# Performance work log

Hardware: AMD Instinct MI355X
Metric: run time of the kernel (lower is better)

Reference implementation:

```python
import jax, jax.numpy as jnp
import numpy as np

LN_EPS = 1e-5

def _lstm_scan(xp, w_hh):
    # xp: [T, B, 4H] precomputed input projections (+bias); w_hh: [4H, H]
    H = w_hh.shape[1]
    B = xp.shape[1]
    def step(carry, x_t):
        h, c = carry
        gates = x_t + h @ w_hh.T
        i, f, g, o = jnp.split(gates, 4, axis=-1)  # torch gate order i,f,g,o
        i = jax.nn.sigmoid(i); f = jax.nn.sigmoid(f)
        g = jnp.tanh(g); o = jax.nn.sigmoid(o)
        c = f * c + i * g
        h = o * jnp.tanh(c)
        return (h, c), h
    init = (jnp.zeros((B, H), xp.dtype), jnp.zeros((B, H), xp.dtype))
    _, hs = jax.lax.scan(step, init, xp)
    return hs  # [T, B, H]

def setup_inputs() -> dict:
    key = jax.random.key(0)
    ks = jax.random.split(key, 16)
    B, T, V, E, K = 64, 512, 21128, 256, 9
    H4 = 4 * E
    s = 0.08  # small init scale for numerical stability
    return {
        'word_ids': jax.random.randint(ks[0], (B, T), 0, V, dtype=jnp.int32),
        'label_ids': jax.random.randint(ks[1], (B, T), 0, K, dtype=jnp.int32),
        'embed_table': jax.random.normal(ks[2], (V, E), jnp.float32) * s,
        'w_ih_f': jax.random.normal(ks[3], (H4, E), jnp.float32) * s,
        'w_hh_f': jax.random.normal(ks[4], (H4, E), jnp.float32) * s,
        'b_f': jnp.zeros((H4,), jnp.float32),
        'w_ih_b': jax.random.normal(ks[5], (H4, E), jnp.float32) * s,
        'w_hh_b': jax.random.normal(ks[6], (H4, E), jnp.float32) * s,
        'b_b': jnp.zeros((H4,), jnp.float32),
        'ln_gamma': jnp.ones((2 * E,), jnp.float32),
        'ln_beta': jnp.zeros((2 * E,), jnp.float32),
        'cls_w': jax.random.normal(ks[7], (K, 2 * E), jnp.float32) * s,
        'cls_b': jnp.zeros((K,), jnp.float32),
        'crf_start': jax.random.normal(ks[8], (K,), jnp.float32) * 0.1,
        'crf_end': jax.random.normal(ks[9], (K,), jnp.float32) * 0.1,
        'crf_trans': jax.random.normal(ks[10], (K, K), jnp.float32) * 0.1,
    }

def reference(word_ids, label_ids, embed_table, w_ih_f, w_hh_f, b_f,
              w_ih_b, w_hh_b, b_b, ln_gamma, ln_beta, cls_w, cls_b,
              crf_start, crf_end, crf_trans):
    # Embedding (dropout is identity at eval)
    emb = embed_table[word_ids]                      # [B, T, E]

    # BiLSTM: precompute input projections once, scan over time
    xf = (emb @ w_ih_f.T + b_f).transpose(1, 0, 2)   # [T, B, 4H]
    hf = _lstm_scan(xf, w_hh_f)                      # [T, B, H]
    xb = (emb[:, ::-1] @ w_ih_b.T + b_b).transpose(1, 0, 2)
    hb = _lstm_scan(xb, w_hh_b)[::-1]                # reverse back to forward time
    seq = jnp.concatenate([hf, hb], axis=-1).transpose(1, 0, 2)  # [B, T, 2H]

    # LayerNorm over last dim
    mu = seq.mean(-1, keepdims=True)
    var = ((seq - mu) ** 2).mean(-1, keepdims=True)
    seq = (seq - mu) * jax.lax.rsqrt(var + LN_EPS) * ln_gamma + ln_beta

    logits = seq @ cls_w.T + cls_b                   # [B, T, K] = CRF emissions

    # --- CRF log-likelihood (no mask: all positions valid) ---
    tags = label_ids
    # numerator: score of gold path
    em_score = jnp.take_along_axis(logits, tags[..., None], axis=-1)[..., 0]  # [B, T]
    trans_score = crf_trans[tags[:, :-1], tags[:, 1:]].sum(axis=1)            # [B]
    numerator = (crf_start[tags[:, 0]] + em_score.sum(axis=1)
                 + trans_score + crf_end[tags[:, -1]])                        # [B]

    # denominator: forward algorithm (logsumexp DP over time)
    alpha0 = crf_start[None, :] + logits[:, 0]       # [B, K]
    em_rest = logits[:, 1:].transpose(1, 0, 2)       # [T-1, B, K]
    def step(alpha, em_t):
        # alpha: [B, K] (prev tag), crf_trans: [K, K], em_t: [B, K] (next tag)
        new = jax.scipy.special.logsumexp(
            alpha[:, :, None] + crf_trans[None, :, :] + em_t[:, None, :], axis=1)
        return new, None
    alpha, _ = jax.lax.scan(step, alpha0, em_rest)
    logZ = jax.scipy.special.logsumexp(alpha + crf_end[None, :], axis=1)      # [B]

    llh = (numerator - logZ).sum()   # torchcrf default reduction='sum'
    loss = -llh
    preds = jnp.argmax(logits, axis=-1)
    return (loss, preds)
```

## Files before the change

### kernel.cpp

```cpp
#include <hip/hip_runtime.h>
#include <cstdint>
#include <cmath>

typedef __attribute__((ext_vector_type(8))) short short8;
typedef __attribute__((ext_vector_type(4))) float floatx4;

__device__ __forceinline__ unsigned pk_bf16(float x, float y) {
    unsigned ux = __float_as_uint(x); ux = ux + 0x7fffu + ((ux >> 16) & 1u);
    unsigned uy = __float_as_uint(y); uy = uy + 0x7fffu + ((uy >> 16) & 1u);
    return (ux >> 16) | (uy & 0xffff0000u);
}
__device__ __forceinline__ unsigned short bf16r(float x) {
    unsigned ux = __float_as_uint(x);
    return (unsigned short)((ux + 0x7fffu + ((ux >> 16) & 1u)) >> 16);
}

__global__ __launch_bounds__(256) void proj_kernel(
    const int* __restrict__ word_ids, const float* __restrict__ embed,
    const float* __restrict__ w_ih_f, const float* __restrict__ b_f,
    const float* __restrict__ w_ih_b, const float* __restrict__ b_b,
    unsigned short* __restrict__ XF, unsigned short* __restrict__ XB,
    int t0, int lgL)
{
    __shared__ unsigned short As[64][264];
    __shared__ unsigned short Bs[64][264];
    __shared__ int idx[64];

    const int tid = threadIdx.x;
    const int jt  = blockIdx.x;
    const int nt  = blockIdx.y;
    const int dir = blockIdx.z;
    const int Lm1 = (1 << lgL) - 1;
    const float* __restrict__ W    = dir ? w_ih_b : w_ih_f;
    const float* __restrict__ bias = dir ? b_b : b_f;
    unsigned short* __restrict__ Xout = dir ? XB : XF;

    if (tid < 64) {
        int n  = nt * 64 + tid;
        int b  = n >> lgL;
        int tl = n & Lm1;
        int tg = dir ? (511 - (t0 + tl)) : (t0 + tl);
        idx[tid] = word_ids[b * 512 + tg];
    }
    __syncthreads();

    #pragma unroll
    for (int i = 0; i < 16; ++i) {
        int flat = i * 256 + tid;
        int r  = flat >> 6;
        int kq = flat & 63;
        floatx4 a = *(const floatx4*)&embed[(size_t)idx[r] * 256 + kq * 4];
        *(uint2*)&As[r][kq * 4] = make_uint2(pk_bf16(a.x, a.y), pk_bf16(a.z, a.w));
        floatx4 wv = *(const floatx4*)&W[(size_t)(jt * 64 + r) * 256 + kq * 4];
        *(uint2*)&Bs[r][kq * 4] = make_uint2(pk_bf16(wv.x, wv.y), pk_bf16(wv.z, wv.w));
    }
    __syncthreads();

    const int w    = tid >> 6;
    const int lane = tid & 63;
    const int q    = lane >> 4;
    const int lr   = lane & 15;

    short8 af[8];
    #pragma unroll
    for (int ks = 0; ks < 8; ++ks)
        af[ks] = *(const short8*)&As[w * 16 + lr][ks * 32 + q * 8];

    floatx4 acc[4];
    #pragma unroll
    for (int jt4 = 0; jt4 < 4; ++jt4) {
        floatx4 c = {0.f, 0.f, 0.f, 0.f};
        #pragma unroll
        for (int ks = 0; ks < 8; ++ks) {
            short8 bf = *(const short8*)&Bs[jt4 * 16 + lr][ks * 32 + q * 8];
            c = __builtin_amdgcn_mfma_f32_16x16x32_bf16(af[ks], bf, c, 0, 0, 0);
        }
        acc[jt4] = c;
    }

    #pragma unroll
    for (int jt4 = 0; jt4 < 4; ++jt4) {
        int j = jt * 64 + jt4 * 16 + lr;
        float bj = bias[j];
        #pragma unroll
        for (int reg = 0; reg < 4; ++reg) {
            int n  = nt * 64 + w * 16 + q * 4 + reg;
            int b  = n >> lgL;
            int tl = n & Lm1;
            Xout[((size_t)tl * 64 + b) * 1024 + j] = bf16r(acc[jt4][reg] + bj);
        }
    }
}

__global__ __launch_bounds__(512, 1) void lstm_scan(
    const unsigned short* __restrict__ XF, const unsigned short* __restrict__ XB,
    const float* __restrict__ w_hh_f, const float* __restrict__ w_hh_b,
    float* __restrict__ hf, float* __restrict__ hb,
    float* __restrict__ state_c, float* __restrict__ state_h, int t0, int t1)
{
    __shared__ unsigned short Ah[2][264];
    __shared__ float scr[4][2][256];
    __shared__ short8 Wlds[8 * 2 * 8 * 64];

    const int blk = blockIdx.x;
    const int dir = blk >> 5;
    const int grp = blk & 31;
    const int B0  = grp * 2;
    const unsigned short* __restrict__ X = dir ? XB : XF;
    const float* __restrict__ Whh = dir ? w_hh_b : w_hh_f;
    float* __restrict__ Hout      = dir ? hb : hf;

    const int tid  = threadIdx.x;
    const int w    = tid >> 6;
    const int lane = tid & 63;
    const int q    = lane >> 4;
    const int lr   = lane & 15;
    const int g    = w >> 1;
    const int uh   = w & 1;

    short8 wreg[6][8];
    #pragma unroll
    for (int ntl = 0; ntl < 8; ++ntl) {
        const float* wrow = &Whh[(size_t)(g * 256 + uh * 128 + ntl * 16 + lr) * 256];
        #pragma unroll
        for (int ks = 0; ks < 8; ++ks) {
            floatx4 a = *(const floatx4*)&wrow[ks * 32 + q * 8];
            floatx4 b = *(const floatx4*)&wrow[ks * 32 + q * 8 + 4];
            union { uint4 u4; short8 s; } cv;
            cv.u4 = make_uint4(pk_bf16(a.x, a.y), pk_bf16(a.z, a.w),
                               pk_bf16(b.x, b.y), pk_bf16(b.z, b.w));
            if (ntl < 6) wreg[ntl][ks] = cv.s;
            else         Wlds[((w * 2 + (ntl - 6)) * 8 + ks) * 64 + lane] = cv.s;
        }
    }

    const int b_p = tid >> 8;
    const int u_p = tid & 255;
    const int sgi = (dir * 64 + B0 + b_p) * 256 + u_p;
    float cst = 0.f;
    float hlast = 0.f;
    if (t0 == 0) {
        Ah[b_p][u_p] = 0;
    } else {
        cst = state_c[sgi];
        hlast = state_h[sgi];
        Ah[b_p][u_p] = bf16r(hlast);
    }

    for (int t = t0; t < t1; ++t) {
        float xg[4];
        {
            const unsigned short* Xc = &X[((size_t)(t - t0) * 64 + B0 + b_p) * 1024 + u_p];
            #pragma unroll
            for (int gg = 0; gg < 4; ++gg)
                xg[gg] = __uint_as_float((unsigned)Xc[gg * 256] << 16);
        }
        __syncthreads();

        short8 af[8];
        #pragma unroll
        for (int ks = 0; ks < 8; ++ks)
            af[ks] = *(const short8*)&Ah[lr & 1][ks * 32 + q * 8];
        #pragma unroll
        for (int ntl = 0; ntl < 8; ++ntl) {
            floatx4 c = {0.f, 0.f, 0.f, 0.f};
            #pragma unroll
            for (int ks = 0; ks < 8; ++ks) {
                short8 bfr = (ntl < 6) ? wreg[ntl][ks]
                           : Wlds[((w * 2 + (ntl - 6)) * 8 + ks) * 64 + lane];
                c = __builtin_amdgcn_mfma_f32_16x16x32_bf16(af[ks], bfr, c, 0, 0, 0);
            }
            if (q == 0) {
                scr[g][0][uh * 128 + ntl * 16 + lr] = c[0];
                scr[g][1][uh * 128 + ntl * 16 + lr] = c[1];
            }
        }
        __syncthreads();

        {
            float gi = scr[0][b_p][u_p] + xg[0];
            float gf = scr[1][b_p][u_p] + xg[1];
            float gg = scr[2][b_p][u_p] + xg[2];
            float go = scr[3][b_p][u_p] + xg[3];
            float ig = 1.f / (1.f + expf(-gi));
            float fg = 1.f / (1.f + expf(-gf));
            float gv = tanhf(gg);
            float og = 1.f / (1.f + expf(-go));
            cst = fg * cst + ig * gv;
            float h = og * tanhf(cst);
            hlast = h;
            int tt = dir ? (511 - t) : t;
            Hout[((size_t)tt * 64 + B0 + b_p) * 256 + u_p] = h;
            Ah[b_p][u_p] = bf16r(h);
        }
    }

    state_c[sgi] = cst;
    state_h[sgi] = hlast;
}

__global__ __launch_bounds__(256) void ln_cls_kernel(
    const float* __restrict__ hf, const float* __restrict__ hb,
    const float* __restrict__ gamma, const float* __restrict__ beta,
    const float* __restrict__ cls_w, const float* __restrict__ cls_b,
    float* __restrict__ logits, float* __restrict__ dout)
{
    const int lane = threadIdx.x & 63;
    const int wid  = threadIdx.x >> 6;
    const int pos  = blockIdx.x * 4 + wid;
    const int b = pos >> 9;
    const int t = pos & 511;

    float4 v0 = *(const float4*)&hf[((size_t)t * 64 + b) * 256 + lane * 4];
    float4 v1 = *(const float4*)&hb[((size_t)t * 64 + b) * 256 + lane * 4];
    float x[8] = {v0.x, v0.y, v0.z, v0.w, v1.x, v1.y, v1.z, v1.w};

    float s = 0.f;
    #pragma unroll
    for (int i = 0; i < 8; ++i) s += x[i];
    #pragma unroll
    for (int off = 32; off > 0; off >>= 1) s += __shfl_xor(s, off, 64);
    float mu = s * (1.f / 512.f);

    float d[8];
    float sq = 0.f;
    #pragma unroll
    for (int i = 0; i < 8; ++i) { d[i] = x[i] - mu; sq += d[i] * d[i]; }
    #pragma unroll
    for (int off = 32; off > 0; off >>= 1) sq += __shfl_xor(sq, off, 64);
    float rs = 1.f / sqrtf(sq * (1.f / 512.f) + 1e-5f);

    float4 g0  = *(const float4*)&gamma[lane * 4];
    float4 g1  = *(const float4*)&gamma[256 + lane * 4];
    float4 be0 = *(const float4*)&beta[lane * 4];
    float4 be1 = *(const float4*)&beta[256 + lane * 4];
    float y[8];
    y[0] = d[0] * rs * g0.x + be0.x; y[1] = d[1] * rs * g0.y + be0.y;
    y[2] = d[2] * rs * g0.z + be0.z; y[3] = d[3] * rs * g0.w + be0.w;
    y[4] = d[4] * rs * g1.x + be1.x; y[5] = d[5] * rs * g1.y + be1.y;
    y[6] = d[6] * rs * g1.z + be1.z; y[7] = d[7] * rs * g1.w + be1.w;

    float lgt[9];
    #pragma unroll
    for (int c = 0; c < 9; ++c) {
        float4 w0 = *(const float4*)&cls_w[c * 512 + lane * 4];
        float4 w1 = *(const float4*)&cls_w[c * 512 + 256 + lane * 4];
        float p = y[0] * w0.x + y[1] * w0.y + y[2] * w0.z + y[3] * w0.w
                + y[4] * w1.x + y[5] * w1.y + y[6] * w1.z + y[7] * w1.w;
        #pragma unroll
        for (int off = 32; off > 0; off >>= 1) p += __shfl_xor(p, off, 64);
        lgt[c] = p + cls_b[c];
    }
    if (lane == 0) {
        int bestc = 0;
        float bestv = lgt[0];
        #pragma unroll
        for (int c = 1; c < 9; ++c)
            if (lgt[c] > bestv) { bestv = lgt[c]; bestc = c; }
        dout[1 + pos] = (float)bestc;
        #pragma unroll
        for (int c = 0; c < 9; ++c) logits[(size_t)pos * 9 + c] = lgt[c];
    }
}

__global__ __launch_bounds__(64) void crf_kernel(
    const float* __restrict__ logits, const int* __restrict__ label_ids,
    const float* __restrict__ crf_start, const float* __restrict__ crf_end,
    const float* __restrict__ crf_trans, float* __restrict__ llh)
{
    __shared__ float Ts[9][12];
    const int b = blockIdx.x;
    const int lane = threadIdx.x;
    if (lane < 81) Ts[lane / 9][lane % 9] = crf_trans[lane];
    __syncthreads();

    const float* __restrict__ em  = &logits[(size_t)b * 512 * 9];
    const int* __restrict__ tags  = &label_ids[b * 512];

    float part = 0.f;
    for (int t = lane; t < 512; t += 64) {
        int tg = tags[t];
        part += em[t * 9 + tg];
        if (t < 511) part += Ts[tg][tags[t + 1]];
    }
    #pragma unroll
    for (int off = 32; off > 0; off >>= 1) part += __shfl_xor(part, off, 64);
    float numer = part + crf_start[tags[0]] + crf_end[tags[511]];

    const int j = (lane < 9) ? lane : 0;
    float alpha = crf_start[j] + em[j];
    for (int t = 1; t < 512; ++t) {
        float av[9];
        float m = -1e30f;
        #pragma unroll
        for (int i = 0; i < 9; ++i) {
            float ai = __shfl(alpha, i, 64);
            av[i] = ai + Ts[i][j];
            m = fmaxf(m, av[i]);
        }
        float ssum = 0.f;
        #pragma unroll
        for (int i = 0; i < 9; ++i) ssum += expf(av[i] - m);
        alpha = m + logf(ssum) + em[t * 9 + j];
    }
    float v = (lane < 9) ? (alpha + crf_end[j]) : -1e30f;
    float mm = v;
    #pragma unroll
    for (int off = 32; off > 0; off >>= 1) mm = fmaxf(mm, __shfl_xor(mm, off, 64));
    float es = (lane < 9) ? expf(v - mm) : 0.f;
    #pragma unroll
    for (int off = 32; off > 0; off >>= 1) es += __shfl_xor(es, off, 64);
    if (lane == 0) llh[b] = numer - (mm + logf(es));
}

__global__ __launch_bounds__(64) void final_reduce(
    const float* __restrict__ llh, float* __restrict__ dout)
{
    float v = llh[threadIdx.x];
    #pragma unroll
    for (int off = 32; off > 0; off >>= 1) v += __shfl_xor(v, off, 64);
    if (threadIdx.x == 0) dout[0] = -v;
}

extern "C" void kernel_launch(void* const* d_in, const int* in_sizes, int n_in,
                              void* d_out, int out_size, void* d_ws, size_t ws_size,
                              hipStream_t stream)
{
    const int*   word_ids  = (const int*)d_in[0];
    const int*   label_ids = (const int*)d_in[1];
    const float* embed     = (const float*)d_in[2];
    const float* w_ih_f    = (const float*)d_in[3];
    const float* w_hh_f    = (const float*)d_in[4];
    const float* b_f       = (const float*)d_in[5];
    const float* w_ih_b    = (const float*)d_in[6];
    const float* w_hh_b    = (const float*)d_in[7];
    const float* b_b       = (const float*)d_in[8];
    const float* ln_gamma  = (const float*)d_in[9];
    const float* ln_beta   = (const float*)d_in[10];
    const float* cls_w     = (const float*)d_in[11];
    const float* cls_b     = (const float*)d_in[12];
    const float* crf_start = (const float*)d_in[13];
    const float* crf_end   = (const float*)d_in[14];
    const float* crf_trans = (const float*)d_in[15];

    char* w = (char*)d_ws;
    auto alloc = [&](size_t bytes) -> char* {
        char* p = w; w += (bytes + 255) & ~(size_t)255; return p;
    };
    float* hf      = (float*)alloc((size_t)8388608 * 4);
    float* hb      = (float*)alloc((size_t)8388608 * 4);
    float* logits  = (float*)alloc((size_t)294912 * 4);
    float* state_c = (float*)alloc((size_t)32768 * 4);
    float* state_h = (float*)alloc((size_t)32768 * 4);
    float* llh     = (float*)alloc((size_t)64 * 4);
    size_t fixed   = (size_t)(w - (char*)d_ws);

    int L = 512;
    while (L > 32 && fixed + (size_t)L * 262144 > ws_size) L >>= 1;
    unsigned short* XF = (unsigned short*)alloc((size_t)L * 65536 * 2);
    unsigned short* XB = (unsigned short*)alloc((size_t)L * 65536 * 2);
    int lgL = 31 - __builtin_clz((unsigned)L);

    for (int t0 = 0; t0 < 512; t0 += L) {
        proj_kernel<<<dim3(16, L, 2), 256, 0, stream>>>(
            word_ids, embed, w_ih_f, b_f, w_ih_b, b_b, XF, XB, t0, lgL);
        lstm_scan<<<64, 512, 0, stream>>>(
            XF, XB, w_hh_f, w_hh_b, hf, hb, state_c, state_h, t0, t0 + L);
    }
    ln_cls_kernel<<<8192, 256, 0, stream>>>(
        hf, hb, ln_gamma, ln_beta, cls_w, cls_b, logits, (float*)d_out);
    crf_kernel<<<64, 64, 0, stream>>>(
        logits, label_ids, crf_start, crf_end, crf_trans, llh);
    final_reduce<<<1, 64, 0, stream>>>(llh, (float*)d_out);
}
```

Before: 1.558 ms.

## Remap LSTM gate columns per wave to drop scratch exchange and one barrier

Reassigns recurrent weight rows so each wave owns all four gates for its 32 hidden units. The gate nonlinearity can then run straight from the MFMA accumulators, with no round trip through a shared scratch buffer. The hidden-state buffer is double-buffered, so each timestep needs one barrier instead of two. Next-step input projections are prefetched into registers, and the occupancy hint changes to waves_per_eu(2,2). In exchange, only half the lanes do the elementwise work, and the MFMA loop issues eight independent accumulators that raise register pressure.

```diff
diff --git a/kernel.cpp b/kernel.cpp
--- a/kernel.cpp
+++ b/kernel.cpp
@@ -13,6 +13,9 @@
 __device__ __forceinline__ unsigned short bf16r(float x) {
     unsigned ux = __float_as_uint(x);
     return (unsigned short)((ux + 0x7fffu + ((ux >> 16) & 1u)) >> 16);
+}
+__device__ __forceinline__ float bf16d(unsigned short v) {
+    return __uint_as_float((unsigned)v << 16);
 }
 
 __global__ __launch_bounds__(256) void proj_kernel(
@@ -92,15 +95,16 @@
     }
 }
 
-__global__ __launch_bounds__(512, 1) void lstm_scan(
+__global__ __launch_bounds__(512)
+__attribute__((amdgpu_waves_per_eu(2, 2)))
+void lstm_scan(
     const unsigned short* __restrict__ XF, const unsigned short* __restrict__ XB,
     const float* __restrict__ w_hh_f, const float* __restrict__ w_hh_b,
     float* __restrict__ hf, float* __restrict__ hb,
     float* __restrict__ state_c, float* __restrict__ state_h, int t0, int t1)
 {
-    __shared__ unsigned short Ah[2][264];
-    __shared__ float scr[4][2][256];
-    __shared__ short8 Wlds[8 * 2 * 8 * 64];
+    __shared__ unsigned short Ah[2][2][264];
+    __shared__ short8 Wlds[8][2][8][64];
 
     const int blk = blockIdx.x;
     const int dir = blk >> 5;
@@ -115,13 +119,12 @@
     const int lane = tid & 63;
     const int q    = lane >> 4;
     const int lr   = lane & 15;
-    const int g    = w >> 1;
-    const int uh   = w & 1;
 
     short8 wreg[6][8];
     #pragma unroll
     for (int ntl = 0; ntl < 8; ++ntl) {
-        const float* wrow = &Whh[(size_t)(g * 256 + uh * 128 + ntl * 16 + lr) * 256];
+        const float* wrow =
+            &Whh[(size_t)((ntl >> 1) * 256 + w * 32 + (ntl & 1) * 16 + lr) * 256];
         #pragma unroll
         for (int ks = 0; ks < 8; ++ks) {
             floatx4 a = *(const floatx4*)&wrow[ks * 32 + q * 8];
@@ -130,73 +133,94 @@
             cv.u4 = make_uint4(pk_bf16(a.x, a.y), pk_bf16(a.z, a.w),
                                pk_bf16(b.x, b.y), pk_bf16(b.z, b.w));
             if (ntl < 6) wreg[ntl][ks] = cv.s;
-            else         Wlds[((w * 2 + (ntl - 6)) * 8 + ks) * 64 + lane] = cv.s;
-        }
-    }
-
-    const int b_p = tid >> 8;
-    const int u_p = tid & 255;
-    const int sgi = (dir * 64 + B0 + b_p) * 256 + u_p;
-    float cst = 0.f;
-    float hlast = 0.f;
+            else         Wlds[w][ntl - 6][ks][lane] = cv.s;
+        }
+    }
+
+    const int u0 = w * 32 + lr;
+    float cst[2] = {0.f, 0.f};
+    float hl[2]  = {0.f, 0.f};
     if (t0 == 0) {
-        Ah[b_p][u_p] = 0;
-    } else {
-        cst = state_c[sgi];
-        hlast = state_h[sgi];
-        Ah[b_p][u_p] = bf16r(hlast);
+        for (int i = tid; i < 528; i += 512) ((unsigned short*)Ah)[i] = 0;
+    } else if (q < 2) {
+        #pragma unroll
+        for (int s = 0; s < 2; ++s) {
+            int sgi = (dir * 64 + B0 + q) * 256 + u0 + s * 16;
+            cst[s] = state_c[sgi];
+            hl[s]  = state_h[sgi];
+            Ah[t0 & 1][q][u0 + s * 16] = bf16r(hl[s]);
+        }
+    }
+
+    unsigned short xc[8];
+    if (q < 2) {
+        const unsigned short* Xc = &X[((size_t)0 * 64 + B0 + q) * 1024];
+        #pragma unroll
+        for (int g = 0; g < 4; ++g)
+            #pragma unroll
+            for (int s = 0; s < 2; ++s)
+                xc[g * 2 + s] = Xc[g * 256 + u0 + s * 16];
     }
 
     for (int t = t0; t < t1; ++t) {
-        float xg[4];
-        {
-            const unsigned short* Xc = &X[((size_t)(t - t0) * 64 + B0 + b_p) * 1024 + u_p];
+        __syncthreads();
+
+        const unsigned short* Asrc = &Ah[t & 1][0][0];
+        floatx4 c0 = {0,0,0,0}, c1 = {0,0,0,0}, c2 = {0,0,0,0}, c3 = {0,0,0,0};
+        floatx4 c4 = {0,0,0,0}, c5 = {0,0,0,0}, c6 = {0,0,0,0}, c7 = {0,0,0,0};
+        #pragma unroll
+        for (int ks = 0; ks < 8; ++ks) {
+            short8 a = *(const short8*)&Asrc[((lr >> 2) & 1) * 264 + ks * 32 + q * 8];
+            short8 w6 = Wlds[w][0][ks][lane];
+            short8 w7 = Wlds[w][1][ks][lane];
+            c0 = __builtin_amdgcn_mfma_f32_16x16x32_bf16(a, wreg[0][ks], c0, 0, 0, 0);
+            c1 = __builtin_amdgcn_mfma_f32_16x16x32_bf16(a, wreg[1][ks], c1, 0, 0, 0);
+            c2 = __builtin_amdgcn_mfma_f32_16x16x32_bf16(a, wreg[2][ks], c2, 0, 0, 0);
+            c3 = __builtin_amdgcn_mfma_f32_16x16x32_bf16(a, wreg[3][ks], c3, 0, 0, 0);
+            c4 = __builtin_amdgcn_mfma_f32_16x16x32_bf16(a, wreg[4][ks], c4, 0, 0, 0);
+            c5 = __builtin_amdgcn_mfma_f32_16x16x32_bf16(a, wreg[5][ks], c5, 0, 0, 0);
+            c6 = __builtin_amdgcn_mfma_f32_16x16x32_bf16(a, w6, c6, 0, 0, 0);
+            c7 = __builtin_amdgcn_mfma_f32_16x16x32_bf16(a, w7, c7, 0, 0, 0);
+        }
+
+        if (q < 2) {
+            int tt = dir ? (511 - t) : t;
+            float pre[8] = {c0[0], c1[0], c2[0], c3[0], c4[0], c5[0], c6[0], c7[0]};
             #pragma unroll
-            for (int gg = 0; gg < 4; ++gg)
-                xg[gg] = __uint_as_float((unsigned)Xc[gg * 256] << 16);
-        }
-        __syncthreads();
-
-        short8 af[8];
-        #pragma unroll
-        for (int ks = 0; ks < 8; ++ks)
-            af[ks] = *(const short8*)&Ah[lr & 1][ks * 32 + q * 8];
-        #pragma unroll
-        for (int ntl = 0; ntl < 8; ++ntl) {
-            floatx4 c = {0.f, 0.f, 0.f, 0.f};
-            #pragma unroll
-            for (int ks = 0; ks < 8; ++ks) {
-                short8 bfr = (ntl < 6) ? wreg[ntl][ks]
-                           : Wlds[((w * 2 + (ntl - 6)) * 8 + ks) * 64 + lane];
-                c = __builtin_amdgcn_mfma_f32_16x16x32_bf16(af[ks], bfr, c, 0, 0, 0);
+            for (int s = 0; s < 2; ++s) {
+                float gi = pre[0 + s] + bf16d(xc[0 + s]);
+                float gf = pre[2 + s] + bf16d(xc[2 + s]);
+                float gg = pre[4 + s] + bf16d(xc[4 + s]);
+                float go = pre[6 + s] + bf16d(xc[6 + s]);
+                float ig = 1.f / (1.f + expf(-gi));
+                float fg = 1.f / (1.f + expf(-gf));
+                float gv = tanhf(gg);
+                float og = 1.f / (1.f + expf(-go));
+                cst[s] = fg * cst[s] + ig * gv;
+                float h = og * tanhf(cst[s]);
+                hl[s] = h;
+                Hout[((size_t)tt * 64 + B0 + q) * 256 + u0 + s * 16] = h;
+                Ah[(t + 1) & 1][q][u0 + s * 16] = bf16r(h);
             }
-            if (q == 0) {
-                scr[g][0][uh * 128 + ntl * 16 + lr] = c[0];
-                scr[g][1][uh * 128 + ntl * 16 + lr] = c[1];
+            if (t + 1 < t1) {
+                const unsigned short* Xc = &X[((size_t)(t + 1 - t0) * 64 + B0 + q) * 1024];
+                #pragma unroll
+                for (int g = 0; g < 4; ++g)
+                    #pragma unroll
+                    for (int s = 0; s < 2; ++s)
+                        xc[g * 2 + s] = Xc[g * 256 + u0 + s * 16];
             }
         }
-        __syncthreads();
-
-        {
-            float gi = scr[0][b_p][u_p] + xg[0];
-            float gf = scr[1][b_p][u_p] + xg[1];
-            float gg = scr[2][b_p][u_p] + xg[2];
-            float go = scr[3][b_p][u_p] + xg[3];
-            float ig = 1.f / (1.f + expf(-gi));
-            float fg = 1.f / (1.f + expf(-gf));
-            float gv = tanhf(gg);
-            float og = 1.f / (1.f + expf(-go));
-            cst = fg * cst + ig * gv;
-            float h = og * tanhf(cst);
-            hlast = h;
-            int tt = dir ? (511 - t) : t;
-            Hout[((size_t)tt * 64 + B0 + b_p) * 256 + u_p] = h;
-            Ah[b_p][u_p] = bf16r(h);
-        }
-    }
-
-    state_c[sgi] = cst;
-    state_h[sgi] = hlast;
+    }
+
+    if (q < 2) {
+        #pragma unroll
+        for (int s = 0; s < 2; ++s) {
+            int sgi = (dir * 64 + B0 + q) * 256 + u0 + s * 16;
+            state_c[sgi] = cst[s];
+            state_h[sgi] = hl[s];
+        }
+    }
 }
 
 __global__ __launch_bounds__(256) void ln_cls_kernel(
```

Result: slower. 2.535 ms (+62.6%).
